# Performance work log

Measured on AMD Instinct MI355X. Metric: run time of the kernel, lower is better.

## Reference

```python
import jax, jax.numpy as jnp
import numpy as np
import math

D_MODEL = 1024
N_DEVICES = 64
HIDDEN = 128
N_HEADS = 8
B, S = 16, 1024
W_SCALE = 0.02

def setup_inputs() -> dict:
    key = jax.random.key(0)
    ks = jax.random.split(key, 24)
    f = jax.random.normal
    inp = {
        'x': f(ks[0], (B, S, D_MODEL), jnp.float32),
        # attention pooling (n_heads=8, non-causal, self-attention) weights, stored [in,out]
        'wq': f(ks[1], (D_MODEL, D_MODEL), jnp.float32) * W_SCALE,
        'bq': jnp.zeros((D_MODEL,), jnp.float32),
        'wk': f(ks[2], (D_MODEL, D_MODEL), jnp.float32) * W_SCALE,
        'bk': jnp.zeros((D_MODEL,), jnp.float32),
        'wv': f(ks[3], (D_MODEL, D_MODEL), jnp.float32) * W_SCALE,
        'bv': jnp.zeros((D_MODEL,), jnp.float32),
        'wo': f(ks[4], (D_MODEL, D_MODEL), jnp.float32) * W_SCALE,
        'bo': jnp.zeros((D_MODEL,), jnp.float32),
        # device embedding table
        'emb': f(ks[5], (N_DEVICES, D_MODEL), jnp.float32),
        # routing gate: Linear(2d,d) -> Tanh -> Linear(d,N) -> Softmax
        'rg_w1': f(ks[6], (2 * D_MODEL, D_MODEL), jnp.float32) * W_SCALE,
        'rg_b1': jnp.zeros((D_MODEL,), jnp.float32),
        'rg_w2': f(ks[7], (D_MODEL, N_DEVICES), jnp.float32) * W_SCALE,
        'rg_b2': jnp.zeros((N_DEVICES,), jnp.float32),
        'reg_w1': f(ks[8], (N_DEVICES, D_MODEL, HIDDEN), jnp.float32) * W_SCALE,
        'reg_b1': jnp.zeros((N_DEVICES, HIDDEN), jnp.float32),
        'reg_w2': f(ks[9], (N_DEVICES, HIDDEN), jnp.float32) * W_SCALE,
        'reg_b2': jnp.zeros((N_DEVICES,), jnp.float32),
        # stacked per-device classification heads: Linear(d,h)->ReLU->Linear(h,1)->Sigmoid
        'cls_w1': f(ks[10], (N_DEVICES, D_MODEL, HIDDEN), jnp.float32) * W_SCALE,
        'cls_b1': jnp.zeros((N_DEVICES, HIDDEN), jnp.float32),
        'cls_w2': f(ks[11], (N_DEVICES, HIDDEN), jnp.float32) * W_SCALE,
        'cls_b2': jnp.zeros((N_DEVICES,), jnp.float32),
    }
    return inp


def _forward(x, wq, bq, wk, bk, wv, bv, wo, bo, emb,
             rg_w1, rg_b1, rg_w2, rg_b2,
             reg_w1, reg_b1, reg_w2, reg_b2,
             cls_w1, cls_b1, cls_w2, cls_b2):
    b, s, d = x.shape
    dk = d // N_HEADS
    scale = 1.0 / math.sqrt(dk)

    def split_heads(t):  # [b,s,d] -> [b,h,s,dk]
        return t.reshape(b, s, N_HEADS, dk).transpose(0, 2, 1, 3)

    Q = split_heads(x @ wq + bq)
    K = split_heads(x @ wk + bk)
    V = split_heads(x @ wv + bv)
    scores = jnp.einsum('bhqd,bhkd->bhqk', Q, K) * scale
    attn = jax.nn.softmax(scores, axis=-1)  # non-causal, no mask, eval (no dropout)
    ctx = jnp.einsum('bhqk,bhkd->bhqd', attn, V)
    ctx = ctx.transpose(0, 2, 1, 3).reshape(b, s, d)
    pooled = ctx @ wo + bo                       # [b,s,d]
    g = pooled.mean(axis=1)                      # [b,d] global_repr

    g_exp = jnp.broadcast_to(g[:, None, :], (b, N_DEVICES, d))
    de_exp = jnp.broadcast_to(emb[None, :, :], (b, N_DEVICES, d))

    # routing gate
    ri = jnp.concatenate([g_exp, de_exp], axis=-1)        # [b,N,2d]
    h = jnp.tanh(ri @ rg_w1 + rg_b1)                      # [b,N,d]
    rw = jax.nn.softmax(h @ rg_w2 + rg_b2, axis=-1)       # [b,N,N]
    device_repr = jnp.einsum('bnm,md->bnd', rw, emb)      # bmm with expanded embeds
    combined = g_exp + device_repr                        # [b,N,d]

    hr = jax.nn.relu(jnp.einsum('bnd,ndh->bnh', combined, reg_w1) + reg_b1)
    reg = jax.nn.softplus(jnp.einsum('bnh,nh->bn', hr, reg_w2) + reg_b2)

    # per-device classification heads (stacked)
    hc = jax.nn.relu(jnp.einsum('bnd,ndh->bnh', combined, cls_w1) + cls_b1)
    cls = jax.nn.sigmoid(jnp.einsum('bnh,nh->bn', hc, cls_w2) + cls_b2)
    return reg, cls


def reference(x, wq, bq, wk, bk, wv, bv, wo, bo, emb,
              rg_w1, rg_b1, rg_w2, rg_b2,
              reg_w1, reg_b1, reg_w2, reg_b2,
              cls_w1, cls_b1, cls_w2, cls_b2):
    return _forward(x, wq, bq, wk, bk, wv, bv, wo, bo, emb,
                    rg_w1, rg_b1, rg_w2, rg_b2,
                    reg_w1, reg_b1, reg_w2, reg_b2,
                    cls_w1, cls_b1, cls_w2, cls_b2)
```

## Files before the change

kernel.cpp:

```cpp
#include <hip/hip_runtime.h>

typedef unsigned short ushort_t;
typedef __attribute__((ext_vector_type(8))) short short8;
typedef __attribute__((ext_vector_type(4))) float floatx4;

__device__ __forceinline__ ushort_t f2bf(float f) {
    unsigned u = __float_as_uint(f);
    return (ushort_t)((u + 0x7fffu + ((u >> 16) & 1u)) >> 16);
}
__device__ __forceinline__ void gll16(const void* g, void* l) {
    __builtin_amdgcn_global_load_lds(
        (const __attribute__((address_space(1))) unsigned int*)g,
        (__attribute__((address_space(3))) unsigned int*)l, 16, 0, 0);
}
#if __has_builtin(__builtin_amdgcn_exp2f)
#define EXP2f(x) __builtin_amdgcn_exp2f(x)
#else
#define EXP2f(x) exp2f(x)
#endif

__global__ __launch_bounds__(256) void prep_tr_kernel(
    const float* __restrict__ x, ushort_t* __restrict__ xb,
    const float* __restrict__ wq, const float* __restrict__ wk,
    ushort_t* __restrict__ wqT, ushort_t* __restrict__ wkT)
{
    __shared__ float t[64][65];
    const int bid = blockIdx.x;
    const int tid = threadIdx.x;
    if (bid < 8192) {
        size_t i = ((size_t)bid * 256 + tid) * 8;
        float4 v0 = *(const float4*)(x + i);
        float4 v1 = *(const float4*)(x + i + 4);
        uint4 o;
        o.x = (unsigned)f2bf(v0.x) | ((unsigned)f2bf(v0.y) << 16);
        o.y = (unsigned)f2bf(v0.z) | ((unsigned)f2bf(v0.w) << 16);
        o.z = (unsigned)f2bf(v1.x) | ((unsigned)f2bf(v1.y) << 16);
        o.w = (unsigned)f2bf(v1.z) | ((unsigned)f2bf(v1.w) << 16);
        *(uint4*)(xb + i) = o;
        return;
    }
    const int b2 = bid - 8192;
    const int bx = b2 & 15, by = (b2 >> 4) & 15, bz = b2 >> 8;
    const float* src = bz ? wk : wq;
    ushort_t* dst = bz ? wkT : wqT;
    const int k0 = bx * 64, n0 = by * 64;
    const int rr = tid >> 4, cc = (tid & 15) * 4;
#pragma unroll
    for (int p = 0; p < 4; ++p) {
        float4 v = *(const float4*)(src + (size_t)(k0 + p * 16 + rr) * 1024 + n0 + cc);
        t[p * 16 + rr][cc + 0] = v.x;
        t[p * 16 + rr][cc + 1] = v.y;
        t[p * 16 + rr][cc + 2] = v.z;
        t[p * 16 + rr][cc + 3] = v.w;
    }
    __syncthreads();
#pragma unroll
    for (int p = 0; p < 4; ++p) {
        int nl = p * 16 + rr;
        uint2 o;
        o.x = (unsigned)f2bf(t[cc + 0][nl]) | ((unsigned)f2bf(t[cc + 1][nl]) << 16);
        o.y = (unsigned)f2bf(t[cc + 2][nl]) | ((unsigned)f2bf(t[cc + 3][nl]) << 16);
        *(uint2*)(dst + (size_t)(n0 + nl) * 1024 + k0 + cc) = o;
    }
}

__global__ __launch_bounds__(512, 4) void gemm_qk_kernel(
    const ushort_t* __restrict__ xb, const ushort_t* __restrict__ wqT, const ushort_t* __restrict__ wkT,
    const float* __restrict__ bq, const float* __restrict__ bk,
    ushort_t* __restrict__ Qb, ushort_t* __restrict__ Kb)
{
    const int bm = blockIdx.x;
    const int bn = blockIdx.y;

    __shared__ ushort_t a_lds[2][128 * 32];
    __shared__ ushort_t q_lds[2][128 * 32];
    __shared__ ushort_t k_lds[2][128 * 32];

    const int tid = threadIdx.x;
    const int lane = tid & 63;
    const int wave = tid >> 6;
    const int wmat = wave >> 2;
    const int wr = (wave >> 1) & 1, wc = wave & 1;
    const int l16 = lane & 15, quad = lane >> 4;
    const int qs = quad ^ ((l16 >> 1) & 3);

    floatx4 acc[4][4];
    const floatx4 zero4 = {0.f, 0.f, 0.f, 0.f};
#pragma unroll
    for (int i = 0; i < 4; ++i)
#pragma unroll
        for (int j = 0; j < 4; ++j) acc[i][j] = zero4;

    const int srow = tid >> 2;
    const int skof = ((tid & 3) ^ ((tid >> 3) & 3)) * 8;
    const ushort_t* gA = xb + (size_t)(bm * 128 + srow) * 1024 + skof;
    const ushort_t* gQ = wqT + (size_t)(bn * 128 + srow) * 1024 + skof;
    const ushort_t* gK = wkT + (size_t)(bn * 128 + srow) * 1024 + skof;

    auto issue = [&](int buf, int k0) {
        gll16(gA + k0, &a_lds[buf][wave * 512]);
        gll16(gQ + k0, &q_lds[buf][wave * 512]);
        gll16(gK + k0, &k_lds[buf][wave * 512]);
    };

    const ushort_t* lbase = wmat ? k_lds[0] : q_lds[0];
    const int lstride = wmat ? (int)(k_lds[1] - k_lds[0]) : (int)(q_lds[1] - q_lds[0]);

    auto compute = [&](int buf) {
        const ushort_t* la = a_lds[buf];
        const ushort_t* lb = lbase + buf * lstride;
        short8 afr[4], bfr[4];
#pragma unroll
        for (int mi = 0; mi < 4; ++mi)
            afr[mi] = *(const short8*)&la[(wr * 64 + mi * 16 + l16) * 32 + qs * 8];
#pragma unroll
        for (int ni = 0; ni < 4; ++ni)
            bfr[ni] = *(const short8*)&lb[(wc * 64 + ni * 16 + l16) * 32 + qs * 8];
#pragma unroll
        for (int mi = 0; mi < 4; ++mi)
#pragma unroll
            for (int ni = 0; ni < 4; ++ni)
                acc[mi][ni] = __builtin_amdgcn_mfma_f32_16x16x32_bf16(afr[mi], bfr[ni], acc[mi][ni], 0, 0, 0);
    };

    issue(0, 0);
#pragma unroll 4
    for (int kt = 0; kt < 31; ++kt) {
        __syncthreads();
        issue((kt + 1) & 1, (kt + 1) * 32);
        compute(kt & 1);
    }
    __syncthreads();
    compute(1);

    ushort_t* Out = wmat ? Kb : Qb;
    const float* bias = wmat ? bk : bq;
    const float postscale = wmat ? 1.0f : 0.12751744900508692f;

    const int bq_ = bm >> 3;
    const int sb = (bm & 7) * 128 + wr * 64 + quad * 4;
    const int dc = wc * 64 + l16;
    float bp[4];
#pragma unroll
    for (int ni = 0; ni < 4; ++ni) bp[ni] = bias[bn * 128 + dc + ni * 16] * postscale;
    ushort_t* ob = Out + ((size_t)(bq_ * 8 + bn) * 1024 + sb) * 128 + dc;
#pragma unroll
    for (int mi = 0; mi < 4; ++mi)
#pragma unroll
        for (int ni = 0; ni < 4; ++ni) {
            ushort_t* p = ob + mi * 2048 + ni * 16;
#pragma unroll
            for (int r = 0; r < 4; ++r)
                p[r * 128] = f2bf(fmaf(acc[mi][ni][r], postscale, bp[ni]));
        }
}

__global__ __launch_bounds__(512, 4) void attn_mfma_kernel(
    const ushort_t* __restrict__ Qb,
    const ushort_t* __restrict__ Kb,
    float* __restrict__ wout)
{
    const int bh = blockIdx.x;
    const int qt = blockIdx.y;
    __shared__ ushort_t ks[2][64 * 128];

    const int tid = threadIdx.x;
    const int wave = tid >> 6, lane = tid & 63;
    const int l16 = lane & 15, quad = lane >> 4;

    const ushort_t* Ksrc = Kb + (size_t)bh * 1024 * 128;

    int srcoff[2];
#pragma unroll
    for (int c = 0; c < 2; ++c) {
        int r = c * 32 + (tid >> 4);
        int g = (tid & 15) ^ (r & 15);
        srcoff[c] = r * 128 + g * 8;
    }

    auto issue = [&](int buf, int kt) {
        const ushort_t* src = Ksrc + (size_t)kt * 8192;
#pragma unroll
        for (int c = 0; c < 2; ++c)
            gll16(src + srcoff[c], &ks[buf][c * 4096 + wave * 512]);
    };

    short8 aq[2][4];
    {
        const ushort_t* qsrc = Qb + ((size_t)bh * 1024 + qt * 256 + wave * 32) * 128;
#pragma unroll
        for (int mi = 0; mi < 2; ++mi)
#pragma unroll
            for (int ksp = 0; ksp < 4; ++ksp)
                aq[mi][ksp] = *(const short8*)(qsrc + (size_t)(mi * 16 + l16) * 128 + ksp * 32 + quad * 8);
    }

    const floatx4 zero4 = {0.f, 0.f, 0.f, 0.f};
    float lsum[2][4];
#pragma unroll
    for (int mi = 0; mi < 2; ++mi)
#pragma unroll
        for (int r = 0; r < 4; ++r) lsum[mi][r] = 0.f;

    issue(0, 0);

    for (int kt = 0; kt < 16; ++kt) {
        __syncthreads();
        if (kt < 15) issue((kt + 1) & 1, kt + 1);
        const ushort_t* kbuf = ks[kt & 1];
        floatx4 acc[2][4];
#pragma unroll
        for (int mi = 0; mi < 2; ++mi)
#pragma unroll
            for (int ni = 0; ni < 4; ++ni) acc[mi][ni] = zero4;
#pragma unroll
        for (int ksp = 0; ksp < 4; ++ksp) {
            short8 bk[4];
#pragma unroll
            for (int ni = 0; ni < 4; ++ni) {
                int n = ni * 16 + l16;
                int gs = (ksp * 4 + quad) ^ (n & 15);
                bk[ni] = *(const short8*)&kbuf[n * 128 + gs * 8];
            }
#pragma unroll
            for (int mi = 0; mi < 2; ++mi)
#pragma unroll
                for (int ni = 0; ni < 4; ++ni)
                    acc[mi][ni] = __builtin_amdgcn_mfma_f32_16x16x32_bf16(aq[mi][ksp], bk[ni], acc[mi][ni], 0, 0, 0);
        }
#pragma unroll
        for (int mi = 0; mi < 2; ++mi)
#pragma unroll
            for (int r = 0; r < 4; ++r) {
                float s = 0.f;
#pragma unroll
                for (int ni = 0; ni < 4; ++ni) s += EXP2f(acc[mi][ni][r]);
                lsum[mi][r] += s;
            }
    }

    issue(0, 0);

    float invl[2][4];
#pragma unroll
    for (int mi = 0; mi < 2; ++mi)
#pragma unroll
        for (int r = 0; r < 4; ++r) {
            float s = lsum[mi][r];
#pragma unroll
            for (int off = 1; off < 16; off <<= 1) s += __shfl_xor(s, off, 16);
            invl[mi][r] = 1.f / s;
        }

    for (int kt = 0; kt < 16; ++kt) {
        __syncthreads();
        if (kt < 15) issue((kt + 1) & 1, kt + 1);
        const ushort_t* kbuf = ks[kt & 1];
        floatx4 acc[2][4];
#pragma unroll
        for (int mi = 0; mi < 2; ++mi)
#pragma unroll
            for (int ni = 0; ni < 4; ++ni) acc[mi][ni] = zero4;
#pragma unroll
        for (int ksp = 0; ksp < 4; ++ksp) {
            short8 bk[4];
#pragma unroll
            for (int ni = 0; ni < 4; ++ni) {
                int n = ni * 16 + l16;
                int gs = (ksp * 4 + quad) ^ (n & 15);
                bk[ni] = *(const short8*)&kbuf[n * 128 + gs * 8];
            }
#pragma unroll
            for (int mi = 0; mi < 2; ++mi)
#pragma unroll
                for (int ni = 0; ni < 4; ++ni)
                    acc[mi][ni] = __builtin_amdgcn_mfma_f32_16x16x32_bf16(aq[mi][ksp], bk[ni], acc[mi][ni], 0, 0, 0);
        }
#pragma unroll
        for (int ni = 0; ni < 4; ++ni) {
            float s = 0.f;
#pragma unroll
            for (int mi = 0; mi < 2; ++mi)
#pragma unroll
                for (int r = 0; r < 4; ++r)
                    s += EXP2f(acc[mi][ni][r]) * invl[mi][r];
            s += __shfl_xor(s, 16, 64);
            s += __shfl_xor(s, 32, 64);
            if (quad == 0) atomicAdd(&wout[bh * 1024 + kt * 64 + ni * 16 + l16], s);
        }
    }
}

__global__ __launch_bounds__(256) void u_kernel(const ushort_t* __restrict__ xb,
                                                const float* __restrict__ w,
                                                float* __restrict__ u)
{
    const int b = blockIdx.x, kc = blockIdx.y;
    const int c4 = threadIdx.x;
    const ushort_t* Xp = xb + ((size_t)(b * 1024 + kc * 64)) * 1024 + c4 * 4;
    float4 acc[8];
#pragma unroll
    for (int h = 0; h < 8; ++h) acc[h] = make_float4(0.f, 0.f, 0.f, 0.f);
    const float* wb = w + b * 8 * 1024 + kc * 64;
    for (int k = 0; k < 64; ++k) {
        uint2 uv = *(const uint2*)(Xp + (size_t)k * 1024);
        float x0 = __uint_as_float(uv.x << 16);
        float x1 = __uint_as_float(uv.x & 0xffff0000u);
        float x2 = __uint_as_float(uv.y << 16);
        float x3 = __uint_as_float(uv.y & 0xffff0000u);
#pragma unroll
        for (int h = 0; h < 8; ++h) {
            float ww = wb[h * 1024 + k];
            acc[h].x = fmaf(ww, x0, acc[h].x);
            acc[h].y = fmaf(ww, x1, acc[h].y);
            acc[h].z = fmaf(ww, x2, acc[h].z);
            acc[h].w = fmaf(ww, x3, acc[h].w);
        }
    }
#pragma unroll
    for (int h = 0; h < 8; ++h) {
        float* dst = u + ((size_t)(b * 8 + h)) * 1024 + c4 * 4;
        atomicAdd(dst + 0, acc[h].x);
        atomicAdd(dst + 1, acc[h].y);
        atomicAdd(dst + 2, acc[h].z);
        atomicAdd(dst + 3, acc[h].w);
    }
}

__global__ __launch_bounds__(256) void sgemm_kernel(
    const float* __restrict__ A, int lda, long sAz,
    const float* __restrict__ Bm, int ldb, long sBz,
    const float* __restrict__ bias, long sBiasz,
    float* __restrict__ C, int ldc, long sCz,
    int M, int N, int K, float alpha, int nks)
{
    const int z = blockIdx.z;
    const int ks = blockIdx.x % nks;
    const int mt = blockIdx.x / nks;
    const int Kc = K / nks;
    A += (size_t)z * sAz;
    Bm += (size_t)z * sBz;
    C += (size_t)z * sCz;
    const float* bptr = bias ? bias + (size_t)z * sBiasz : nullptr;
    __shared__ float As[64 * 36];
    __shared__ float Bs[32 * 68];
    const int tid = threadIdx.x;
    const int row0 = mt * 64, col0 = blockIdx.y * 64;
    const int ty = tid >> 4, tx = tid & 15;
    float acc[4][4] = {};
    const int aflat = tid * 8;
    const int ar = aflat >> 5, ac = aflat & 31;
    const int br = aflat >> 6, bc = aflat & 63;
    for (int k0 = ks * Kc; k0 < (ks + 1) * Kc; k0 += 32) {
        __syncthreads();
        float4 va0 = make_float4(0.f, 0.f, 0.f, 0.f), va1 = va0;
        if (row0 + ar < M) {
            const float* src = A + (size_t)(row0 + ar) * lda + k0 + ac;
            va0 = *(const float4*)src;
            va1 = *(const float4*)(src + 4);
        }
        *(float4*)&As[ar * 36 + ac] = va0;
        *(float4*)&As[ar * 36 + ac + 4] = va1;
        {
            const float* srcb = Bm + (size_t)(k0 + br) * ldb + col0 + bc;
            *(float4*)&Bs[br * 68 + bc] = *(const float4*)srcb;
            *(float4*)&Bs[br * 68 + bc + 4] = *(const float4*)(srcb + 4);
        }
        __syncthreads();
#pragma unroll
        for (int kk = 0; kk < 32; ++kk) {
            float a0 = As[(ty * 4 + 0) * 36 + kk];
            float a1 = As[(ty * 4 + 1) * 36 + kk];
            float a2 = As[(ty * 4 + 2) * 36 + kk];
            float a3 = As[(ty * 4 + 3) * 36 + kk];
            float b0 = Bs[kk * 68 + tx * 4 + 0];
            float b1 = Bs[kk * 68 + tx * 4 + 1];
            float b2 = Bs[kk * 68 + tx * 4 + 2];
            float b3 = Bs[kk * 68 + tx * 4 + 3];
            acc[0][0] = fmaf(a0, b0, acc[0][0]); acc[0][1] = fmaf(a0, b1, acc[0][1]);
            acc[0][2] = fmaf(a0, b2, acc[0][2]); acc[0][3] = fmaf(a0, b3, acc[0][3]);
            acc[1][0] = fmaf(a1, b0, acc[1][0]); acc[1][1] = fmaf(a1, b1, acc[1][1]);
            acc[1][2] = fmaf(a1, b2, acc[1][2]); acc[1][3] = fmaf(a1, b3, acc[1][3]);
            acc[2][0] = fmaf(a2, b0, acc[2][0]); acc[2][1] = fmaf(a2, b1, acc[2][1]);
            acc[2][2] = fmaf(a2, b2, acc[2][2]); acc[2][3] = fmaf(a2, b3, acc[2][3]);
            acc[3][0] = fmaf(a3, b0, acc[3][0]); acc[3][1] = fmaf(a3, b1, acc[3][1]);
            acc[3][2] = fmaf(a3, b2, acc[3][2]); acc[3][3] = fmaf(a3, b3, acc[3][3]);
        }
    }
#pragma unroll
    for (int i = 0; i < 4; ++i) {
        int r = row0 + ty * 4 + i;
        if (r >= M) continue;
#pragma unroll
        for (int j = 0; j < 4; ++j) {
            int c = col0 + tx * 4 + j;
            float v = alpha * acc[i][j] + ((bptr && ks == 0) ? bptr[c] : 0.f);
            if (nks > 1) atomicAdd(&C[(size_t)r * ldc + c], v);
            else C[(size_t)r * ldc + c] = v;
        }
    }
}

__global__ __launch_bounds__(256) void sgemm_ge_ee_kernel(
    const float* __restrict__ gbuf, const float* __restrict__ emb,
    const float* __restrict__ rg_w1, float* __restrict__ Ge, float* __restrict__ Ee)
{
    const int z = blockIdx.z;
    const float* A = z ? emb : gbuf;
    const float* Bm = rg_w1 + (size_t)z * 1048576;
    float* C = z ? Ee : Ge;
    const int M = z ? 64 : 16;
    const int nks = 8, Kc = 128;
    const int ks = blockIdx.x % nks;
    __shared__ float As[64 * 36];
    __shared__ float Bs[32 * 68];
    const int tid = threadIdx.x;
    const int col0 = blockIdx.y * 64;
    const int ty = tid >> 4, tx = tid & 15;
    float acc[4][4] = {};
    const int aflat = tid * 8;
    const int ar = aflat >> 5, ac = aflat & 31;
    const int br = aflat >> 6, bc = aflat & 63;
    for (int k0 = ks * Kc; k0 < (ks + 1) * Kc; k0 += 32) {
        __syncthreads();
        float4 va0 = make_float4(0.f, 0.f, 0.f, 0.f), va1 = va0;
        if (ar < M) {
            const float* src = A + (size_t)ar * 1024 + k0 + ac;
            va0 = *(const float4*)src;
            va1 = *(const float4*)(src + 4);
        }
        *(float4*)&As[ar * 36 + ac] = va0;
        *(float4*)&As[ar * 36 + ac + 4] = va1;
        {
            const float* srcb = Bm + (size_t)(k0 + br) * 1024 + col0 + bc;
            *(float4*)&Bs[br * 68 + bc] = *(const float4*)srcb;
            *(float4*)&Bs[br * 68 + bc + 4] = *(const float4*)(srcb + 4);
        }
        __syncthreads();
#pragma unroll
        for (int kk = 0; kk < 32; ++kk) {
            float a0 = As[(ty * 4 + 0) * 36 + kk];
            float a1 = As[(ty * 4 + 1) * 36 + kk];
            float a2 = As[(ty * 4 + 2) * 36 + kk];
            float a3 = As[(ty * 4 + 3) * 36 + kk];
            float b0 = Bs[kk * 68 + tx * 4 + 0];
            float b1 = Bs[kk * 68 + tx * 4 + 1];
            float b2 = Bs[kk * 68 + tx * 4 + 2];
            float b3 = Bs[kk * 68 + tx * 4 + 3];
            acc[0][0] = fmaf(a0, b0, acc[0][0]); acc[0][1] = fmaf(a0, b1, acc[0][1]);
            acc[0][2] = fmaf(a0, b2, acc[0][2]); acc[0][3] = fmaf(a0, b3, acc[0][3]);
            acc[1][0] = fmaf(a1, b0, acc[1][0]); acc[1][1] = fmaf(a1, b1, acc[1][1]);
            acc[1][2] = fmaf(a1, b2, acc[1][2]); acc[1][3] = fmaf(a1, b3, acc[1][3]);
            acc[2][0] = fmaf(a2, b0, acc[2][0]); acc[2][1] = fmaf(a2, b1, acc[2][1]);
            acc[2][2] = fmaf(a2, b2, acc[2][2]); acc[2][3] = fmaf(a2, b3, acc[2][3]);
            acc[3][0] = fmaf(a3, b0, acc[3][0]); acc[3][1] = fmaf(a3, b1, acc[3][1]);
            acc[3][2] = fmaf(a3, b2, acc[3][2]); acc[3][3] = fmaf(a3, b3, acc[3][3]);
        }
    }
#pragma unroll
    for (int i = 0; i < 4; ++i) {
        int r = ty * 4 + i;
        if (r >= M) continue;
#pragma unroll
        for (int j = 0; j < 4; ++j) {
            int c = col0 + tx * 4 + j;
            atomicAdd(&C[(size_t)r * 1024 + c], acc[i][j]);
        }
    }
}

__global__ __launch_bounds__(256) void gate_kernel(
    const float* __restrict__ Ge, const float* __restrict__ Ee, const float* __restrict__ rg_b1,
    const float* __restrict__ rg_w2, const float* __restrict__ rg_b2,
    const float* __restrict__ emb, float* __restrict__ DR)
{
    const int row = blockIdx.x;
    const int b = row >> 6, n = row & 63;
    __shared__ float h[1024];
    __shared__ float red[256];
    __shared__ float rw[64];
    const int tid = threadIdx.x;
    for (int c = tid; c < 1024; c += 256)
        h[c] = tanhf(Ge[b * 1024 + c] + Ee[n * 1024 + c] + rg_b1[c]);
    __syncthreads();
    const int j = tid & 63, ch = tid >> 6;
    float part = 0.f;
    const float* w2p = rg_w2 + (size_t)(ch * 256) * 64 + j;
    for (int c = 0; c < 256; ++c)
        part = fmaf(h[ch * 256 + c], w2p[c * 64], part);
    red[tid] = part;
    __syncthreads();
    if (tid < 64) {
        float lg = red[tid] + red[tid + 64] + red[tid + 128] + red[tid + 192] + rg_b2[j];
        float m = lg;
#pragma unroll
        for (int off = 1; off < 64; off <<= 1) m = fmaxf(m, __shfl_xor(m, off, 64));
        float e = __expf(lg - m);
        float s = e;
#pragma unroll
        for (int off = 1; off < 64; off <<= 1) s += __shfl_xor(s, off, 64);
        rw[tid] = e / s;
    }
    __syncthreads();
    float4 acc = make_float4(0.f, 0.f, 0.f, 0.f);
    const float4* E4 = (const float4*)emb;
    for (int nn = 0; nn < 64; ++nn) {
        float wv = rw[nn];
        float4 ev = E4[nn * 256 + tid];
        acc.x = fmaf(wv, ev.x, acc.x);
        acc.y = fmaf(wv, ev.y, acc.y);
        acc.z = fmaf(wv, ev.z, acc.z);
        acc.w = fmaf(wv, ev.w, acc.w);
    }
    *(float4*)&DR[(size_t)row * 1024 + tid * 4] = acc;
}

__global__ __launch_bounds__(256) void heads_p1_kernel(
    const float* __restrict__ g, const float* __restrict__ DR,
    const float* __restrict__ rw1, const float* __restrict__ cw1,
    float* __restrict__ hpart)
{
    const int n = blockIdx.x, task = blockIdx.y, ksl = blockIdx.z;
    __shared__ float combs[16 * 128];
    const int tid = threadIdx.x;
    for (int i = tid; i < 2048; i += 256) {
        int b = i >> 7, c = i & 127;
        int gc = ksl * 128 + c;
        combs[i] = g[b * 1024 + gc] + DR[((size_t)(b * 64 + n)) * 1024 + gc];
    }
    __syncthreads();
    const int j = tid & 127, sub = tid >> 7;
    const float* W1 = (task ? cw1 : rw1) + (size_t)n * 131072 + (size_t)ksl * 128 * 128;
    float a[8] = {};
    for (int c4 = 0; c4 < 32; ++c4) {
        const float w0 = W1[(c4 * 4 + 0) * 128 + j];
        const float w1 = W1[(c4 * 4 + 1) * 128 + j];
        const float w2 = W1[(c4 * 4 + 2) * 128 + j];
        const float w3 = W1[(c4 * 4 + 3) * 128 + j];
#pragma unroll
        for (int bb = 0; bb < 8; ++bb) {
            float4 cv = *(const float4*)&combs[(sub * 8 + bb) * 128 + c4 * 4];
            a[bb] = fmaf(cv.x, w0, a[bb]);
            a[bb] = fmaf(cv.y, w1, a[bb]);
            a[bb] = fmaf(cv.z, w2, a[bb]);
            a[bb] = fmaf(cv.w, w3, a[bb]);
        }
    }
    float* dst = hpart + (((size_t)(ksl * 2 + task) * 64 + n) * 16 + sub * 8) * 128 + j;
#pragma unroll
    for (int bb = 0; bb < 8; ++bb) dst[bb * 128] = a[bb];
}

__global__ __launch_bounds__(256) void heads_p2_kernel(
    const float* __restrict__ hpart,
    const float* __restrict__ rb1, const float* __restrict__ rw2, const float* __restrict__ rb2,
    const float* __restrict__ cb1, const float* __restrict__ cw2, const float* __restrict__ cb2,
    float* __restrict__ out)
{
    const int n = blockIdx.x, task = blockIdx.y;
    const int tid = threadIdx.x;
    const int b = tid >> 4, jg = tid & 15;
    const float* b1 = (task ? cb1 : rb1) + n * 128 + jg * 8;
    const float* W2 = (task ? cw2 : rw2) + n * 128 + jg * 8;
    float s = 0.f;
#pragma unroll
    for (int k = 0; k < 8; ++k) {
        float h = b1[k];
#pragma unroll
        for (int ksl = 0; ksl < 8; ++ksl)
            h += hpart[(((size_t)(ksl * 2 + task) * 64 + n) * 16 + b) * 128 + jg * 8 + k];
        s = fmaf(fmaxf(h, 0.f), W2[k], s);
    }
#pragma unroll
    for (int off = 1; off < 16; off <<= 1) s += __shfl_xor(s, off, 16);
    if (jg == 0) {
        s += (task ? cb2 : rb2)[n];
        float r = task ? (1.f / (1.f + __expf(-s)))
                       : (fmaxf(s, 0.f) + log1pf(__expf(-fabsf(s))));
        out[task * 1024 + b * 64 + n] = r;
    }
}

extern "C" void kernel_launch(void* const* d_in, const int* in_sizes, int n_in,
                              void* d_out, int out_size, void* d_ws, size_t ws_size,
                              hipStream_t stream)
{
    const float* x      = (const float*)d_in[0];
    const float* wq     = (const float*)d_in[1];
    const float* bq     = (const float*)d_in[2];
    const float* wk     = (const float*)d_in[3];
    const float* bk     = (const float*)d_in[4];
    const float* wv     = (const float*)d_in[5];
    const float* bv     = (const float*)d_in[6];
    const float* wo     = (const float*)d_in[7];
    const float* bo     = (const float*)d_in[8];
    const float* emb    = (const float*)d_in[9];
    const float* rg_w1  = (const float*)d_in[10];
    const float* rg_b1  = (const float*)d_in[11];
    const float* rg_w2  = (const float*)d_in[12];
    const float* rg_b2  = (const float*)d_in[13];
    const float* reg_w1 = (const float*)d_in[14];
    const float* reg_b1 = (const float*)d_in[15];
    const float* reg_w2 = (const float*)d_in[16];
    const float* reg_b2 = (const float*)d_in[17];
    const float* cls_w1 = (const float*)d_in[18];
    const float* cls_b1 = (const float*)d_in[19];
    const float* cls_w2 = (const float*)d_in[20];
    const float* cls_b2 = (const float*)d_in[21];

    char* ws = (char*)d_ws;
    size_t off = 0;
    auto alloc = [&](size_t bytes) { size_t cur = off; off += (bytes + 255) & ~(size_t)255; return cur; };

    ushort_t* xb  = (ushort_t*)(ws + alloc((size_t)16777216 * 2));
    ushort_t* wqT = (ushort_t*)(ws + alloc((size_t)1048576 * 2));
    ushort_t* wkT = (ushort_t*)(ws + alloc((size_t)1048576 * 2));
    ushort_t* Qb  = (ushort_t*)(ws + alloc((size_t)16777216 * 2));
    ushort_t* Kb  = (ushort_t*)(ws + alloc((size_t)16777216 * 2));
    size_t zero_beg = off;
    float* wcol = (float*)(ws + alloc((size_t)131072 * 4));
    float* u    = (float*)(ws + alloc((size_t)131072 * 4));
    float* cm   = (float*)(ws + alloc((size_t)16384 * 4));
    float* gbuf = (float*)(ws + alloc((size_t)16384 * 4));
    float* Ge   = (float*)(ws + alloc((size_t)16384 * 4));
    float* Ee   = (float*)(ws + alloc((size_t)65536 * 4));
    size_t zero_end = off;
    float* DR    = (float*)(ws + alloc((size_t)1048576 * 4));
    float* hpart = (float*)(ws + alloc((size_t)2097152 * 4));

    hipMemsetAsync(ws + zero_beg, 0, zero_end - zero_beg, stream);

    prep_tr_kernel<<<8704, 256, 0, stream>>>(x, xb, wq, wk, wqT, wkT);
    gemm_qk_kernel<<<dim3(128, 8), 512, 0, stream>>>(xb, wqT, wkT, bq, bk, Qb, Kb);
    attn_mfma_kernel<<<dim3(128, 4), 512, 0, stream>>>(Qb, Kb, wcol);
    u_kernel<<<dim3(16, 16), 256, 0, stream>>>(xb, wcol, u);
    sgemm_kernel<<<dim3(4, 2, 8), 256, 0, stream>>>(u, 8192, 1024, wv, 1024, 128, bv, 128,
                                                    cm, 1024, 128, 16, 128, 1024, 1.f / 1024.f, 4);
    sgemm_kernel<<<dim3(8, 16, 1), 256, 0, stream>>>(cm, 1024, 0, wo, 1024, 0, bo, 0,
                                                     gbuf, 1024, 0, 16, 1024, 1024, 1.f, 8);
    sgemm_ge_ee_kernel<<<dim3(8, 16, 2), 256, 0, stream>>>(gbuf, emb, rg_w1, Ge, Ee);
    gate_kernel<<<1024, 256, 0, stream>>>(Ge, Ee, rg_b1, rg_w2, rg_b2, emb, DR);
    heads_p1_kernel<<<dim3(64, 2, 8), 256, 0, stream>>>(gbuf, DR, reg_w1, cls_w1, hpart);
    heads_p2_kernel<<<dim3(64, 2), 256, 0, stream>>>(hpart, reg_b1, reg_w2, reg_b2,
                                                     cls_b1, cls_w2, cls_b2, (float*)d_out);
    (void)in_sizes; (void)n_in; (void)out_size; (void)ws_size;
}
```

Measured before the change: 487.0 us.

## Deepen QK GEMM LDS pipeline to four stages with explicit vmcnt waits

Expands the QK projection GEMM's LDS staging from double to quadruple buffering, keeping three K-tiles of async global-to-LDS loads in flight. Each iteration waits on vmcnt with a raw barrier instead of a full __syncthreads drain, so memory latency overlaps the MFMA work. LDS use doubles to 48KB per block, so launch bounds drop from 4 to 2 blocks per CU, which may reduce occupancy. Correctness now relies on hand-counted vmcnt values.

```diff
diff --git a/kernel.cpp b/kernel.cpp
--- a/kernel.cpp
+++ b/kernel.cpp
@@ -64,7 +64,7 @@
     }
 }
 
-__global__ __launch_bounds__(512, 4) void gemm_qk_kernel(
+__global__ __launch_bounds__(512, 2) void gemm_qk_kernel(
     const ushort_t* __restrict__ xb, const ushort_t* __restrict__ wqT, const ushort_t* __restrict__ wkT,
     const float* __restrict__ bq, const float* __restrict__ bk,
     ushort_t* __restrict__ Qb, ushort_t* __restrict__ Kb)
@@ -72,9 +72,9 @@
     const int bm = blockIdx.x;
     const int bn = blockIdx.y;
 
-    __shared__ ushort_t a_lds[2][128 * 32];
-    __shared__ ushort_t q_lds[2][128 * 32];
-    __shared__ ushort_t k_lds[2][128 * 32];
+    __shared__ ushort_t a_lds[4][128 * 32];
+    __shared__ ushort_t q_lds[4][128 * 32];
+    __shared__ ushort_t k_lds[4][128 * 32];
 
     const int tid = threadIdx.x;
     const int lane = tid & 63;
@@ -97,18 +97,18 @@
     const ushort_t* gQ = wqT + (size_t)(bn * 128 + srow) * 1024 + skof;
     const ushort_t* gK = wkT + (size_t)(bn * 128 + srow) * 1024 + skof;
 
-    auto issue = [&](int buf, int k0) {
+    auto issue = [&](int s) {
+        const int buf = s & 3;
+        const int k0 = s * 32;
         gll16(gA + k0, &a_lds[buf][wave * 512]);
         gll16(gQ + k0, &q_lds[buf][wave * 512]);
         gll16(gK + k0, &k_lds[buf][wave * 512]);
     };
 
-    const ushort_t* lbase = wmat ? k_lds[0] : q_lds[0];
-    const int lstride = wmat ? (int)(k_lds[1] - k_lds[0]) : (int)(q_lds[1] - q_lds[0]);
-
-    auto compute = [&](int buf) {
+    auto compute = [&](int s) {
+        const int buf = s & 3;
         const ushort_t* la = a_lds[buf];
-        const ushort_t* lb = lbase + buf * lstride;
+        const ushort_t* lb = wmat ? k_lds[buf] : q_lds[buf];
         short8 afr[4], bfr[4];
 #pragma unroll
         for (int mi = 0; mi < 4; ++mi)
@@ -123,15 +123,27 @@
                 acc[mi][ni] = __builtin_amdgcn_mfma_f32_16x16x32_bf16(afr[mi], bfr[ni], acc[mi][ni], 0, 0, 0);
     };
 
-    issue(0, 0);
+    issue(0); issue(1); issue(2);
 #pragma unroll 4
-    for (int kt = 0; kt < 31; ++kt) {
-        __syncthreads();
-        issue((kt + 1) & 1, (kt + 1) * 32);
-        compute(kt & 1);
-    }
-    __syncthreads();
-    compute(1);
+    for (int kt = 0; kt < 29; ++kt) {
+        asm volatile("s_waitcnt vmcnt(6)" ::: "memory");
+        __builtin_amdgcn_s_barrier();
+        __builtin_amdgcn_sched_barrier(0);
+        issue(kt + 3);
+        compute(kt);
+    }
+    asm volatile("s_waitcnt vmcnt(6)" ::: "memory");
+    __builtin_amdgcn_s_barrier();
+    __builtin_amdgcn_sched_barrier(0);
+    compute(29);
+    asm volatile("s_waitcnt vmcnt(3)" ::: "memory");
+    __builtin_amdgcn_s_barrier();
+    __builtin_amdgcn_sched_barrier(0);
+    compute(30);
+    asm volatile("s_waitcnt vmcnt(0)" ::: "memory");
+    __builtin_amdgcn_s_barrier();
+    __builtin_amdgcn_sched_barrier(0);
+    compute(31);
 
     ushort_t* Out = wmat ? Kb : Qb;
     const float* bias = wmat ? bk : bq;
```

Result: slower. 519.1 us (+6.6%).

## Reduce u in shared memory and fuse the two head kernels

Applied to the files above, without the earlier changes.

u_kernel now gives each block a 64-column slice and reduces partial sums across the 16 k-chunks in shared memory, so it writes u directly instead of issuing atomics. That lets u move out of the memset region. The two head kernels become one that splits the full 1024-wide reduction across two halves, combines them in LDS and applies the second linear layer plus activation in the same block, which removes the hpart round trip and one launch. The sgemm split-K for cm rises from 4 to 8. The trade-off is that each head block now reads 128 KB of W1 rows per batch quad, so weights are re-read 4 times, and parallelism in the head stage is lower.

```diff
diff --git a/kernel.cpp b/kernel.cpp
--- a/kernel.cpp
+++ b/kernel.cpp
@@ -295,13 +295,18 @@
                                                 const float* __restrict__ w,
                                                 float* __restrict__ u)
 {
-    const int b = blockIdx.x, kc = blockIdx.y;
-    const int c4 = threadIdx.x;
-    const ushort_t* Xp = xb + ((size_t)(b * 1024 + kc * 64)) * 1024 + c4 * 4;
+    const int b = blockIdx.x, dc = blockIdx.y;
+    const int tid = threadIdx.x;
+    const int kp = tid >> 4, dli = tid & 15;
+    const int d0 = dc * 64;
+    __shared__ float4 accl[16][8][16];
+
     float4 acc[8];
 #pragma unroll
     for (int h = 0; h < 8; ++h) acc[h] = make_float4(0.f, 0.f, 0.f, 0.f);
-    const float* wb = w + b * 8 * 1024 + kc * 64;
+
+    const ushort_t* Xp = xb + ((size_t)(b * 1024 + kp * 64)) * 1024 + d0 + dli * 4;
+    const float* wb = w + b * 8192 + kp * 64;
     for (int k = 0; k < 64; ++k) {
         uint2 uv = *(const uint2*)(Xp + (size_t)k * 1024);
         float x0 = __uint_as_float(uv.x << 16);
@@ -318,12 +323,17 @@
         }
     }
 #pragma unroll
-    for (int h = 0; h < 8; ++h) {
-        float* dst = u + ((size_t)(b * 8 + h)) * 1024 + c4 * 4;
-        atomicAdd(dst + 0, acc[h].x);
-        atomicAdd(dst + 1, acc[h].y);
-        atomicAdd(dst + 2, acc[h].z);
-        atomicAdd(dst + 3, acc[h].w);
+    for (int h = 0; h < 8; ++h) accl[kp][h][dli] = acc[h];
+    __syncthreads();
+    if (tid < 128) {
+        const int h = tid >> 4, di = tid & 15;
+        float4 s = accl[0][h][di];
+#pragma unroll
+        for (int k2 = 1; k2 < 16; ++k2) {
+            float4 v = accl[k2][h][di];
+            s.x += v.x; s.y += v.y; s.z += v.z; s.w += v.w;
+        }
+        *(float4*)&u[((size_t)(b * 8 + h)) * 1024 + d0 + di * 4] = s;
     }
 }
 
@@ -515,69 +525,61 @@
     *(float4*)&DR[(size_t)row * 1024 + tid * 4] = acc;
 }
 
-__global__ __launch_bounds__(256) void heads_p1_kernel(
+__global__ __launch_bounds__(256) void heads_kernel(
     const float* __restrict__ g, const float* __restrict__ DR,
     const float* __restrict__ rw1, const float* __restrict__ cw1,
-    float* __restrict__ hpart)
-{
-    const int n = blockIdx.x, task = blockIdx.y, ksl = blockIdx.z;
-    __shared__ float combs[16 * 128];
-    const int tid = threadIdx.x;
-    for (int i = tid; i < 2048; i += 256) {
-        int b = i >> 7, c = i & 127;
-        int gc = ksl * 128 + c;
-        combs[i] = g[b * 1024 + gc] + DR[((size_t)(b * 64 + n)) * 1024 + gc];
+    const float* __restrict__ rb1, const float* __restrict__ rw2, const float* __restrict__ rb2,
+    const float* __restrict__ cb1, const float* __restrict__ cw2, const float* __restrict__ cb2,
+    float* __restrict__ out)
+{
+    const int n = blockIdx.x, task = blockIdx.y, bq = blockIdx.z;
+    __shared__ float comb[4][1024];
+    __shared__ float apart[2][4][128];
+    const int tid = threadIdx.x;
+#pragma unroll
+    for (int i = 0; i < 4; ++i) {
+        int idx = tid + i * 256;
+        int bb = idx >> 8, c4 = idx & 255;
+        int b = bq * 4 + bb;
+        float4 gv = *(const float4*)&g[b * 1024 + c4 * 4];
+        float4 dv = *(const float4*)&DR[((size_t)(b * 64 + n)) * 1024 + c4 * 4];
+        *(float4*)&comb[bb][c4 * 4] = make_float4(gv.x + dv.x, gv.y + dv.y, gv.z + dv.z, gv.w + dv.w);
     }
     __syncthreads();
     const int j = tid & 127, sub = tid >> 7;
-    const float* W1 = (task ? cw1 : rw1) + (size_t)n * 131072 + (size_t)ksl * 128 * 128;
-    float a[8] = {};
-    for (int c4 = 0; c4 < 32; ++c4) {
-        const float w0 = W1[(c4 * 4 + 0) * 128 + j];
-        const float w1 = W1[(c4 * 4 + 1) * 128 + j];
-        const float w2 = W1[(c4 * 4 + 2) * 128 + j];
-        const float w3 = W1[(c4 * 4 + 3) * 128 + j];
-#pragma unroll
-        for (int bb = 0; bb < 8; ++bb) {
-            float4 cv = *(const float4*)&combs[(sub * 8 + bb) * 128 + c4 * 4];
+    const float* W1 = (task ? cw1 : rw1) + (size_t)n * 131072 + (size_t)sub * 512 * 128 + j;
+    float a[4] = {};
+    for (int c4 = 0; c4 < 128; ++c4) {
+        const int cb = sub * 512 + c4 * 4;
+        const float w0 = W1[(c4 * 4 + 0) * 128];
+        const float w1 = W1[(c4 * 4 + 1) * 128];
+        const float w2 = W1[(c4 * 4 + 2) * 128];
+        const float w3 = W1[(c4 * 4 + 3) * 128];
+#pragma unroll
+        for (int bb = 0; bb < 4; ++bb) {
+            float4 cv = *(const float4*)&comb[bb][cb];
             a[bb] = fmaf(cv.x, w0, a[bb]);
             a[bb] = fmaf(cv.y, w1, a[bb]);
             a[bb] = fmaf(cv.z, w2, a[bb]);
             a[bb] = fmaf(cv.w, w3, a[bb]);
         }
     }
-    float* dst = hpart + (((size_t)(ksl * 2 + task) * 64 + n) * 16 + sub * 8) * 128 + j;
-#pragma unroll
-    for (int bb = 0; bb < 8; ++bb) dst[bb * 128] = a[bb];
-}
-
-__global__ __launch_bounds__(256) void heads_p2_kernel(
-    const float* __restrict__ hpart,
-    const float* __restrict__ rb1, const float* __restrict__ rw2, const float* __restrict__ rb2,
-    const float* __restrict__ cb1, const float* __restrict__ cw2, const float* __restrict__ cb2,
-    float* __restrict__ out)
-{
-    const int n = blockIdx.x, task = blockIdx.y;
-    const int tid = threadIdx.x;
-    const int b = tid >> 4, jg = tid & 15;
-    const float* b1 = (task ? cb1 : rb1) + n * 128 + jg * 8;
-    const float* W2 = (task ? cw2 : rw2) + n * 128 + jg * 8;
-    float s = 0.f;
-#pragma unroll
-    for (int k = 0; k < 8; ++k) {
-        float h = b1[k];
-#pragma unroll
-        for (int ksl = 0; ksl < 8; ++ksl)
-            h += hpart[(((size_t)(ksl * 2 + task) * 64 + n) * 16 + b) * 128 + jg * 8 + k];
-        s = fmaf(fmaxf(h, 0.f), W2[k], s);
-    }
-#pragma unroll
-    for (int off = 1; off < 16; off <<= 1) s += __shfl_xor(s, off, 16);
-    if (jg == 0) {
+#pragma unroll
+    for (int bb = 0; bb < 4; ++bb) apart[sub][bb][j] = a[bb];
+    __syncthreads();
+    const int wv = tid >> 6, lane = tid & 63;
+    const float* b1 = (task ? cb1 : rb1) + n * 128;
+    const float* W2 = (task ? cw2 : rw2) + n * 128;
+    float h1 = b1[lane]      + apart[0][wv][lane]      + apart[1][wv][lane];
+    float h2 = b1[lane + 64] + apart[0][wv][lane + 64] + apart[1][wv][lane + 64];
+    float s = fmaxf(h1, 0.f) * W2[lane] + fmaxf(h2, 0.f) * W2[lane + 64];
+#pragma unroll
+    for (int off = 1; off < 64; off <<= 1) s += __shfl_xor(s, off, 64);
+    if (lane == 0) {
         s += (task ? cb2 : rb2)[n];
         float r = task ? (1.f / (1.f + __expf(-s)))
                        : (fmaxf(s, 0.f) + log1pf(__expf(-fabsf(s))));
-        out[task * 1024 + b * 64 + n] = r;
+        out[task * 1024 + (bq * 4 + wv) * 64 + n] = r;
     }
 }
 
@@ -619,14 +621,13 @@
     ushort_t* Kb  = (ushort_t*)(ws + alloc((size_t)16777216 * 2));
     size_t zero_beg = off;
     float* wcol = (float*)(ws + alloc((size_t)131072 * 4));
-    float* u    = (float*)(ws + alloc((size_t)131072 * 4));
     float* cm   = (float*)(ws + alloc((size_t)16384 * 4));
     float* gbuf = (float*)(ws + alloc((size_t)16384 * 4));
     float* Ge   = (float*)(ws + alloc((size_t)16384 * 4));
     float* Ee   = (float*)(ws + alloc((size_t)65536 * 4));
     size_t zero_end = off;
-    float* DR    = (float*)(ws + alloc((size_t)1048576 * 4));
-    float* hpart = (float*)(ws + alloc((size_t)2097152 * 4));
+    float* u    = (float*)(ws + alloc((size_t)131072 * 4));
+    float* DR   = (float*)(ws + alloc((size_t)1048576 * 4));
 
     hipMemsetAsync(ws + zero_beg, 0, zero_end - zero_beg, stream);
 
@@ -634,14 +635,14 @@
     gemm_qk_kernel<<<dim3(128, 8), 512, 0, stream>>>(xb, wqT, wkT, bq, bk, Qb, Kb);
     attn_mfma_kernel<<<dim3(128, 4), 512, 0, stream>>>(Qb, Kb, wcol);
     u_kernel<<<dim3(16, 16), 256, 0, stream>>>(xb, wcol, u);
-    sgemm_kernel<<<dim3(4, 2, 8), 256, 0, stream>>>(u, 8192, 1024, wv, 1024, 128, bv, 128,
-                                                    cm, 1024, 128, 16, 128, 1024, 1.f / 1024.f, 4);
+    sgemm_kernel<<<dim3(8, 2, 8), 256, 0, stream>>>(u, 8192, 1024, wv, 1024, 128, bv, 128,
+                                                    cm, 1024, 128, 16, 128, 1024, 1.f / 1024.f, 8);
     sgemm_kernel<<<dim3(8, 16, 1), 256, 0, stream>>>(cm, 1024, 0, wo, 1024, 0, bo, 0,
                                                      gbuf, 1024, 0, 16, 1024, 1024, 1.f, 8);
     sgemm_ge_ee_kernel<<<dim3(8, 16, 2), 256, 0, stream>>>(gbuf, emb, rg_w1, Ge, Ee);
     gate_kernel<<<1024, 256, 0, stream>>>(Ge, Ee, rg_b1, rg_w2, rg_b2, emb, DR);
-    heads_p1_kernel<<<dim3(64, 2, 8), 256, 0, stream>>>(gbuf, DR, reg_w1, cls_w1, hpart);
-    heads_p2_kernel<<<dim3(64, 2), 256, 0, stream>>>(hpart, reg_b1, reg_w2, reg_b2,
+    heads_kernel<<<dim3(64, 2, 4), 256, 0, stream>>>(gbuf, DR, reg_w1, cls_w1,
+                                                     reg_b1, reg_w2, reg_b2,
                                                      cls_b1, cls_w2, cls_b2, (float*)d_out);
     (void)in_sizes; (void)n_in; (void)out_size; (void)ws_size;
 }
```

Result: faster. 452.8 us (-7.0%).
